# Optimization experiments

Hardware: AMD Instinct MI355X
Metric: run time of the kernel (lower is better)

## Reference

```python
import jax, jax.numpy as jnp
import numpy as np

WS = 16          # window_size
N = WS * WS      # tokens per window
H = 8            # num_heads
HD = 64          # head_dim
DIM = 512
EPEG_K = 15
PAD = EPEG_K // 2


def _relative_position_index(ws):
    coords = np.stack(np.meshgrid(np.arange(ws), np.arange(ws), indexing='ij'))  # (2, ws, ws)
    flat = coords.reshape(2, -1)                                                 # (2, N)
    rel = flat[:, :, None] - flat[:, None, :]                                    # (2, N, N)
    rel = rel.transpose(1, 2, 0).astype(np.int64)                                # (N, N, 2)
    rel[..., 0] += ws - 1
    rel[..., 1] += ws - 1
    rel[..., 0] *= 2 * ws - 1
    return rel.sum(-1)                                                           # (N, N)

REL_IDX = jnp.asarray(_relative_position_index(WS), dtype=jnp.int32)


def setup_inputs() -> dict:
    key = jax.random.key(0)
    ks = jax.random.split(key, 8)
    B_ = 128
    x = jax.random.normal(ks[0], (B_, N, DIM), dtype=jnp.float32)
    qkv_w = jax.random.normal(ks[1], (3 * H * HD, DIM), dtype=jnp.float32) * 0.02
    qkv_b = jnp.zeros((3 * H * HD,), dtype=jnp.float32)
    pe_w = jax.random.normal(ks[2], (H, 1, EPEG_K, 1), dtype=jnp.float32) * 0.02  # depthwise (15,1) conv
    pe_b = jnp.zeros((H,), dtype=jnp.float32)
    rpb_table = jax.random.normal(ks[3], ((2 * WS - 1) * (2 * WS - 1), H), dtype=jnp.float32) * 0.02
    proj_w = jax.random.normal(ks[4], (DIM, H * HD), dtype=jnp.float32) * 0.02
    proj_b = jnp.zeros((DIM,), dtype=jnp.float32)
    return {"x": x, "qkv_w": qkv_w, "qkv_b": qkv_b, "pe_w": pe_w, "pe_b": pe_b,
            "rpb_table": rpb_table, "proj_w": proj_w, "proj_b": proj_b}


def reference(x, qkv_w, qkv_b, pe_w, pe_b, rpb_table, proj_w, proj_b):
    B_, n, _ = x.shape
    scale = HD ** -0.5
    qkv = (x @ qkv_w.T + qkv_b).reshape(B_, n, 3, H, HD).transpose(2, 0, 3, 1, 4)  # (3,B_,H,N,hd)
    q, k, v = qkv[0] * scale, qkv[1], qkv[2]
    attn = jnp.einsum('bhnd,bhmd->bhnm', q, k)                                    # (B_,H,N,N)
    # epeg: depthwise conv (k,1) over the score map, per head
    pe = jax.lax.conv_general_dilated(
        attn, pe_w, window_strides=(1, 1), padding=((PAD, PAD), (0, 0)),
        dimension_numbers=('NCHW', 'OIHW', 'NCHW'), feature_group_count=H)
    attn = attn + pe + pe_b[None, :, None, None]
    bias = rpb_table[REL_IDX.reshape(-1)].reshape(n, n, H).transpose(2, 0, 1)     # (H,N,N)
    attn = jax.nn.softmax(attn + bias[None], axis=-1)
    out = jnp.einsum('bhnm,bhmd->bnhd', attn, v).reshape(B_, n, H * HD)
    return out @ proj_w.T + proj_b
```

## Files before the change

kernel.cpp:

```cpp
#include <hip/hip_runtime.h>


typedef unsigned short u16;
typedef unsigned int u32;
typedef __attribute__((ext_vector_type(8))) short short8;
typedef __attribute__((ext_vector_type(4))) float f32x4;

__device__ __forceinline__ u16 f2bf(float f) {
  union { float f; u32 u; } v; v.f = f;
  return (u16)((v.u + 0x7FFFu + ((v.u >> 16) & 1u)) >> 16);
}
__device__ __forceinline__ float bf2f(u16 s) {
  union { u32 u; float f; } v; v.u = ((u32)s) << 16;
  return v.f;
}
__device__ __forceinline__ u32 cvtpk(float lo, float hi) {
  u32 r;
  asm("v_cvt_pk_bf16_f32 %0, %1, %2" : "=v"(r) : "v"(lo), "v"(hi));
  return r;
}

__device__ __forceinline__ void gl2lds16(const u16* g, u16* l) {
  __builtin_amdgcn_global_load_lds((const __attribute__((address_space(1))) void*)g,
                                   (__attribute__((address_space(3))) void*)l, 16, 0, 0);
}

__device__ __forceinline__ int fragaddr(int frag, int lane) {
  return (frag * 64 + (lane ^ (frag & 7))) * 8;
}

__global__ __launch_bounds__(256) void cvt_all(
    const float* __restrict__ x, const float* __restrict__ w1f,
    const float* __restrict__ w2f, u16* __restrict__ xo,
    u16* __restrict__ w1o, u16* __restrict__ w2o) {
  const int NX = 4194304, NW1 = 196608, NW2 = 65536;
  int i = blockIdx.x * 256 + threadIdx.x;
  const float* src; u16* dst; int j;
  if (i < NX)                  { src = x;   dst = xo;  j = i; }
  else if (i < NX + NW1)       { src = w1f; dst = w1o; j = i - NX; }
  else if (i < NX + NW1 + NW2) { src = w2f; dst = w2o; j = i - NX - NW1; }
  else return;
  float4 f = ((const float4*)src)[j];
  uint2 o;
  o.x = (u32)f2bf(f.x) | ((u32)f2bf(f.y) << 16);
  o.y = (u32)f2bf(f.z) | ((u32)f2bf(f.w) << 16);
  ((uint2*)dst)[j] = o;
}

__device__ __forceinline__ void gemm256_core(
    const u16* __restrict__ A, const u16* __restrict__ B,
    int m0, int n0, u16* lds, f32x4 acc[8][4]) {
  const int NT = 8;
  int tid = threadIdx.x, wave = tid >> 6, lane = tid & 63;
  int wm = wave >> 2, wn = wave & 3;

  int ch0 = tid, ch1 = tid + 512;
  int row0 = ch0 >> 2, row1 = ch1 >> 2;
  int cg0 = (ch0 & 3) ^ (row0 & 3) ^ ((row0 >> 2) & 3);
  int cg1 = (ch1 & 3) ^ (row1 & 3) ^ ((row1 >> 2) & 3);
  const u16* Ag0 = A + (size_t)(m0 + row0) * 512 + cg0 * 8;
  const u16* Ag1 = A + (size_t)(m0 + row1) * 512 + cg1 * 8;
  const u16* Bg0 = B + (size_t)(n0 + row0) * 512 + cg0 * 8;
  const u16* Bg1 = B + (size_t)(n0 + row1) * 512 + cg1 * 8;
  int ldsu0 = wave * 64 * 8;
  int ldsu1 = (512 + wave * 64) * 8;

  int frag_off = (lane & 15) * 32 +
                 (((lane >> 4) ^ (lane & 3) ^ ((lane >> 2) & 3)) << 3);
  int abase = wm * 4096 + frag_off;
  int bbase = 8192 + wn * 2048 + frag_off;

#define STAGE(h)                                                             \
  do {                                                                       \
    if ((h) < NT * 4) {                                                      \
      int T_ = (h) >> 2, kh_ = ((h) >> 1) & 1, isB_ = (h) & 1;               \
      int ko_ = T_ * 64 + kh_ * 32;                                          \
      u16* d_ = lds + (T_ & 1) * 32768 + kh_ * 16384 + isB_ * 8192;          \
      gl2lds16((isB_ ? Bg0 : Ag0) + ko_, d_ + ldsu0);                        \
      gl2lds16((isB_ ? Bg1 : Ag1) + ko_, d_ + ldsu1);                        \
    }                                                                        \
  } while (0)

#define LDA(dst, mf, kh, p)                                                  \
  dst = *(const short8*)(lds + (p) * 32768 + (kh) * 16384 + abase + (mf) * 512)
#define LDB(dst, nf, kh, p)                                                  \
  dst = *(const short8*)(lds + (p) * 32768 + (kh) * 16384 + bbase + (nf) * 512)

#define MM16(M0)                                                                                   \
  __builtin_amdgcn_s_setprio(1);                                                                   \
  acc[(M0)+0][0] = __builtin_amdgcn_mfma_f32_16x16x32_bf16(b0, a0, acc[(M0)+0][0], 0, 0, 0);       \
  acc[(M0)+0][1] = __builtin_amdgcn_mfma_f32_16x16x32_bf16(b1, a0, acc[(M0)+0][1], 0, 0, 0);       \
  acc[(M0)+0][2] = __builtin_amdgcn_mfma_f32_16x16x32_bf16(b2, a0, acc[(M0)+0][2], 0, 0, 0);       \
  acc[(M0)+0][3] = __builtin_amdgcn_mfma_f32_16x16x32_bf16(b3, a0, acc[(M0)+0][3], 0, 0, 0);       \
  acc[(M0)+1][0] = __builtin_amdgcn_mfma_f32_16x16x32_bf16(b0, a1, acc[(M0)+1][0], 0, 0, 0);       \
  acc[(M0)+1][1] = __builtin_amdgcn_mfma_f32_16x16x32_bf16(b1, a1, acc[(M0)+1][1], 0, 0, 0);       \
  acc[(M0)+1][2] = __builtin_amdgcn_mfma_f32_16x16x32_bf16(b2, a1, acc[(M0)+1][2], 0, 0, 0);       \
  acc[(M0)+1][3] = __builtin_amdgcn_mfma_f32_16x16x32_bf16(b3, a1, acc[(M0)+1][3], 0, 0, 0);       \
  acc[(M0)+2][0] = __builtin_amdgcn_mfma_f32_16x16x32_bf16(b0, a2, acc[(M0)+2][0], 0, 0, 0);       \
  acc[(M0)+2][1] = __builtin_amdgcn_mfma_f32_16x16x32_bf16(b1, a2, acc[(M0)+2][1], 0, 0, 0);       \
  acc[(M0)+2][2] = __builtin_amdgcn_mfma_f32_16x16x32_bf16(b2, a2, acc[(M0)+2][2], 0, 0, 0);       \
  acc[(M0)+2][3] = __builtin_amdgcn_mfma_f32_16x16x32_bf16(b3, a2, acc[(M0)+2][3], 0, 0, 0);       \
  acc[(M0)+3][0] = __builtin_amdgcn_mfma_f32_16x16x32_bf16(b0, a3, acc[(M0)+3][0], 0, 0, 0);       \
  acc[(M0)+3][1] = __builtin_amdgcn_mfma_f32_16x16x32_bf16(b1, a3, acc[(M0)+3][1], 0, 0, 0);       \
  acc[(M0)+3][2] = __builtin_amdgcn_mfma_f32_16x16x32_bf16(b2, a3, acc[(M0)+3][2], 0, 0, 0);       \
  acc[(M0)+3][3] = __builtin_amdgcn_mfma_f32_16x16x32_bf16(b3, a3, acc[(M0)+3][3], 0, 0, 0);       \
  __builtin_amdgcn_s_setprio(0)

  STAGE(0); STAGE(1); STAGE(2); STAGE(3); STAGE(4);
  asm volatile("s_waitcnt vmcnt(6)" ::: "memory");
  __builtin_amdgcn_s_barrier();

#pragma unroll 1
  for (int kt = 0; kt < NT; ++kt) {
    int p = kt & 1;
    int hb = kt * 4 + 5;
    short8 a0, a1, a2, a3, b0, b1, b2, b3;
    LDA(a0, 0, 0, p); LDA(a1, 1, 0, p); LDA(a2, 2, 0, p); LDA(a3, 3, 0, p);
    LDB(b0, 0, 0, p); LDB(b1, 1, 0, p); LDB(b2, 2, 0, p); LDB(b3, 3, 0, p);
    STAGE(hb);
    __builtin_amdgcn_s_barrier();
    asm volatile("s_waitcnt lgkmcnt(0)" ::: "memory");
    MM16(0);
    __builtin_amdgcn_s_barrier();
    LDA(a0, 4, 0, p); LDA(a1, 5, 0, p); LDA(a2, 6, 0, p); LDA(a3, 7, 0, p);
    STAGE(hb + 1);
    __builtin_amdgcn_s_barrier();
    asm volatile("s_waitcnt lgkmcnt(0)" ::: "memory");
    MM16(4);
    if (kt == NT - 1) asm volatile("s_waitcnt vmcnt(0)" ::: "memory");
    else              asm volatile("s_waitcnt vmcnt(6)" ::: "memory");
    __builtin_amdgcn_s_barrier();
    LDA(a0, 0, 1, p); LDA(a1, 1, 1, p); LDA(a2, 2, 1, p); LDA(a3, 3, 1, p);
    LDB(b0, 0, 1, p); LDB(b1, 1, 1, p); LDB(b2, 2, 1, p); LDB(b3, 3, 1, p);
    STAGE(hb + 2);
    __builtin_amdgcn_s_barrier();
    asm volatile("s_waitcnt lgkmcnt(0)" ::: "memory");
    MM16(0);
    __builtin_amdgcn_s_barrier();
    LDA(a0, 4, 1, p); LDA(a1, 5, 1, p); LDA(a2, 6, 1, p); LDA(a3, 7, 1, p);
    STAGE(hb + 3);
    __builtin_amdgcn_s_barrier();
    asm volatile("s_waitcnt lgkmcnt(0)" ::: "memory");
    MM16(4);
    if (kt == NT - 2)     asm volatile("s_waitcnt vmcnt(4)" ::: "memory");
    else if (kt < NT - 2) asm volatile("s_waitcnt vmcnt(6)" ::: "memory");
    __builtin_amdgcn_s_barrier();
  }
#undef STAGE
#undef LDA
#undef LDB
#undef MM16
}

__global__ __launch_bounds__(512, 2) void gemm_qkv256(
    const u16* __restrict__ A, const u16* __restrict__ B,
    const float* __restrict__ qkvb, u16* __restrict__ qb,
    u16* __restrict__ kb, u16* __restrict__ vb) {
  __shared__ __align__(16) u16 lds[65536];
  f32x4 acc[8][4];
#pragma unroll
  for (int a = 0; a < 8; ++a)
#pragma unroll
    for (int c = 0; c < 4; ++c) acc[a][c] = (f32x4){0.f, 0.f, 0.f, 0.f};
  int bid = blockIdx.x;
  int wg = (bid & 7) * 96 + (bid >> 3);
  int m0 = (wg / 6) * 256, n0 = (wg % 6) * 256;
  gemm256_core(A, B, m0, n0, lds, acc);

  int tid = threadIdx.x, wave = tid >> 6, lane = tid & 63;
  int wm = wave >> 2, wn = wave & 3;
  int cx = lane & 15, g = lane >> 4;

  __syncthreads();
  float sc = (n0 < 512) ? 0.125f : 1.f;
  float4 bvn[4];
#pragma unroll
  for (int nf = 0; nf < 4; ++nf)
    bvn[nf] = *(const float4*)(qkvb + n0 + wn * 64 + nf * 16 + g * 4);
#pragma unroll
  for (int mf = 0; mf < 8; ++mf) {
    int r = wm * 128 + mf * 16 + cx;
    int swz = r & 7;
#pragma unroll
    for (int nf = 0; nf < 4; ++nf) {
      int c0 = wn * 64 + nf * 16 + g * 4;
      int c16 = (c0 >> 3) ^ swz;
      f32x4 v = acc[mf][nf];
      u32 w0 = cvtpk((v[0] + bvn[nf].x) * sc, (v[1] + bvn[nf].y) * sc);
      u32 w1 = cvtpk((v[2] + bvn[nf].z) * sc, (v[3] + bvn[nf].w) * sc);
      *(uint2*)(lds + r * 256 + c16 * 8 + (c0 & 7)) = make_uint2(w0, w1);
    }
  }
  __syncthreads();

  int b = m0 >> 8;
  int nrow = tid >> 3, dc = tid & 7;
#pragma unroll
  for (int j = 0; j < 16; ++j) {
    const int hg = j >> 2;
    int gcol = n0 + hg * 64;
    int which = gcol >> 9;
    int h = (gcol >> 6) & 7;
    u16* dst = (which == 0 ? qb : (which == 1 ? kb : vb)) +
               (size_t)(b * 8 + h) * 16384;
    int n = (j & 3) * 64 + nrow;
    int c16 = (hg * 8 + dc) ^ (n & 7);
    uint4 val = *(const uint4*)(lds + n * 256 + c16 * 8);
    *(uint4*)(dst + n * 64 + dc * 8) = val;
  }
}

__global__ __launch_bounds__(512, 2) void gemm_proj256(
    const u16* __restrict__ A, const u16* __restrict__ B,
    const float* __restrict__ pb, float* __restrict__ out) {
  __shared__ __align__(16) u16 lds[65536];
  f32x4 acc[8][4];
#pragma unroll
  for (int a = 0; a < 8; ++a)
#pragma unroll
    for (int c = 0; c < 4; ++c) acc[a][c] = (f32x4){0.f, 0.f, 0.f, 0.f};
  int bid = blockIdx.x;
  int wg = (bid & 7) * 32 + (bid >> 3);
  int m0 = (wg >> 1) * 256, n0 = (wg & 1) * 256;
  gemm256_core(A, B, m0, n0, lds, acc);

  int tid = threadIdx.x, wave = tid >> 6, lane = tid & 63;
  int wm = wave >> 2, wn = wave & 3;
  int cx = lane & 15, g = lane >> 4;
  int cb = n0 + wn * 64 + g * 4;
  float4 bv[4];
#pragma unroll
  for (int nf = 0; nf < 4; ++nf) bv[nf] = *(const float4*)(pb + cb + nf * 16);
  int r0 = m0 + wm * 128 + cx;
#pragma unroll
  for (int mf = 0; mf < 8; ++mf) {
    size_t rb = (size_t)(r0 + mf * 16) * 512;
#pragma unroll
    for (int nf = 0; nf < 4; ++nf) {
      f32x4 v = acc[mf][nf];
      float4 o = make_float4(v[0] + bv[nf].x, v[1] + bv[nf].y,
                             v[2] + bv[nf].z, v[3] + bv[nf].w);
      *(float4*)(out + rb + cb + nf * 16) = o;
    }
  }
}

__global__ __launch_bounds__(256) void qconv(u16* __restrict__ qb,
                                             const float* __restrict__ pe_w) {
  __shared__ __align__(16) u16 Ql[256 * 72];
  __shared__ float w[15];
  int bh = blockIdx.x, h = bh & 7, tid = threadIdx.x;
  const uint4* src = (const uint4*)(qb + (size_t)bh * 16384);
#pragma unroll
  for (int it = 0; it < 8; ++it) {
    int idx = tid + it * 256;
    int row = idx >> 3, c = (idx & 7) * 8;
    *(uint4*)(Ql + row * 72 + c) = src[idx];
  }
  if (tid < 15) w[tid] = pe_w[h * 15 + tid] + (tid == 7 ? 1.f : 0.f);
  __syncthreads();
  int dg = (tid & 15) * 4, nb4 = tid >> 4;
  uint2* dst = (uint2*)(qb + (size_t)bh * 16384);
#pragma unroll
  for (int i = 0; i < 16; ++i) {
    int n = nb4 + i * 16;
    float a0 = 0.f, a1 = 0.f, a2 = 0.f, a3 = 0.f;
#pragma unroll
    for (int t = 0; t < 15; ++t) {
      int nn = n + t - 7;
      if (nn < 0 || nn > 255) continue;
      uint2 rv = *(const uint2*)(Ql + nn * 72 + dg);
      float wt = w[t];
      a0 += wt * bf2f(rv.x & 0xffff); a1 += wt * bf2f(rv.x >> 16);
      a2 += wt * bf2f(rv.y & 0xffff); a3 += wt * bf2f(rv.y >> 16);
    }
    uint2 pv;
    pv.x = (u32)f2bf(a0) | ((u32)f2bf(a1) << 16);
    pv.y = (u32)f2bf(a2) | ((u32)f2bf(a3) << 16);
    dst[(n * 64 + dg) >> 2] = pv;
  }
}

__global__ __launch_bounds__(512, 2) void attn_win(
    const u16* __restrict__ qb, const u16* __restrict__ kb,
    const u16* __restrict__ vb, const float* __restrict__ pe_b,
    const float* __restrict__ rpb, u16* __restrict__ attnout) {
  __shared__ __align__(16) u16 KfPs[21504];
  __shared__ __align__(16) u16 Vf[16384];
  __shared__ float biasl[961];

  int bh = blockIdx.x, b = bh >> 3, h = bh & 7;
  int tid = threadIdx.x, wave = tid >> 6, lane = tid & 63;
  int cx = lane & 15, g = lane >> 4;

  const uint4* kg = (const uint4*)(kb + (size_t)bh * 16384);
  const uint4* vg = (const uint4*)(vb + (size_t)bh * 16384);
  const u16* qgb = qb + (size_t)bh * 16384;

  short8 qfr0a = *(const short8*)(qgb + (0 * 128 + wave * 16 + cx) * 64 + g * 8);
  short8 qfr0b = *(const short8*)(qgb + (0 * 128 + wave * 16 + cx) * 64 + 32 + g * 8);
  short8 qfr1a = *(const short8*)(qgb + (1 * 128 + wave * 16 + cx) * 64 + g * 8);
  short8 qfr1b = *(const short8*)(qgb + (1 * 128 + wave * 16 + cx) * 64 + 32 + g * 8);

  uint4 kreg[4];
#pragma unroll
  for (int it = 0; it < 4; ++it) kreg[it] = kg[tid + it * 512];

  u16* Vtmp = KfPs;
#pragma unroll
  for (int it = 0; it < 4; ++it) {
    int idx = tid + it * 512;
    uint4 v = vg[idx];
    int row = idx >> 3, c8 = (idx & 7) * 8;
    *(uint2*)(Vtmp + row * 68 + c8)     = make_uint2(v.x, v.y);
    *(uint2*)(Vtmp + row * 68 + c8 + 4) = make_uint2(v.z, v.w);
  }
  {
    float peb = pe_b[h];
    for (int i = tid; i < 961; i += 512) biasl[i] = rpb[i * 8 + h] + peb;
  }
  __syncthreads();

#pragma unroll
  for (int it = 0; it < 4; ++it) {
    int o = tid + it * 512;
    int frag = o >> 6, lanep = o & 63;
    int d = (frag >> 3) * 16 + (lanep & 15);
    int mb = (frag & 7) * 32 + (lanep >> 4) * 8;
    uint4 pk;
    pk.x = (u32)Vtmp[(mb + 0) * 68 + d] | ((u32)Vtmp[(mb + 1) * 68 + d] << 16);
    pk.y = (u32)Vtmp[(mb + 2) * 68 + d] | ((u32)Vtmp[(mb + 3) * 68 + d] << 16);
    pk.z = (u32)Vtmp[(mb + 4) * 68 + d] | ((u32)Vtmp[(mb + 5) * 68 + d] << 16);
    pk.w = (u32)Vtmp[(mb + 6) * 68 + d] | ((u32)Vtmp[(mb + 7) * 68 + d] << 16);
    *(uint4*)(Vf + (frag * 64 + (lanep ^ (frag & 7))) * 8) = pk;
  }
  __syncthreads();

  u16* Kf = KfPs;
#pragma unroll
  for (int it = 0; it < 4; ++it) {
    int idx = tid + it * 512;
    int n = idx >> 3, k8 = idx & 7;
    int frag = (n >> 4) * 2 + (k8 >> 2);
    int lanep = (n & 15) + 16 * (k8 & 3);
    *(uint4*)(Kf + (frag * 64 + (lanep ^ (frag & 7))) * 8) = kreg[it];
  }
  __syncthreads();

  u16* Psw = KfPs + 16384 + wave * 640;

#pragma unroll
  for (int it2 = 0; it2 < 2; ++it2) {
    short8 qf0 = it2 ? qfr1a : qfr0a;
    short8 qf1 = it2 ? qfr1b : qfr0b;
    int qbase = it2 * 128 + wave * 16;

    float m_run = -1e30f, l_run = 0.f;
    f32x4 oacc[4];
#pragma unroll
    for (int dt = 0; dt < 4; ++dt) oacc[dt] = (f32x4){0.f, 0.f, 0.f, 0.f};

#pragma unroll
    for (int c = 0; c < 2; ++c) {
      f32x4 acc[8];
#pragma unroll
      for (int mt = 0; mt < 8; ++mt) acc[mt] = (f32x4){0.f, 0.f, 0.f, 0.f};
      __builtin_amdgcn_s_setprio(1);
#pragma unroll
      for (int mt = 0; mt < 8; ++mt) {
        int fr = (c * 8 + mt) * 2;
        short8 k0 = *(const short8*)(Kf + fragaddr(fr, lane));
        short8 k1 = *(const short8*)(Kf + fragaddr(fr + 1, lane));
        acc[mt] = __builtin_amdgcn_mfma_f32_16x16x32_bf16(k0, qf0, acc[mt], 0, 0, 0);
        acc[mt] = __builtin_amdgcn_mfma_f32_16x16x32_bf16(k1, qf1, acc[mt], 0, 0, 0);
      }
      __builtin_amdgcn_s_setprio(0);

      int nb = (it2 * 8 + wave - c * 8 + 15) * 31 + cx - g * 4 + 15;
#pragma unroll
      for (int mt = 0; mt < 8; ++mt) {
        const float* bp = biasl + (nb - 31 * mt);
        acc[mt][0] += bp[0];  acc[mt][1] += bp[-1];
        acc[mt][2] += bp[-2]; acc[mt][3] += bp[-3];
      }

      float mx = fmaxf(fmaxf(acc[0][0], acc[0][1]), fmaxf(acc[0][2], acc[0][3]));
#pragma unroll
      for (int mt = 1; mt < 8; ++mt)
        mx = fmaxf(mx, fmaxf(fmaxf(acc[mt][0], acc[mt][1]),
                             fmaxf(acc[mt][2], acc[mt][3])));
      mx = fmaxf(mx, __shfl_xor(mx, 16));
      mx = fmaxf(mx, __shfl_xor(mx, 32));
      float mnew = fmaxf(m_run, mx);
      float al = __expf(m_run - mnew);
      float s = 0.f;
#pragma unroll
      for (int mt = 0; mt < 8; ++mt)
#pragma unroll
        for (int i = 0; i < 4; ++i) {
          float e = __expf(acc[mt][i] - mnew);
          acc[mt][i] = e; s += e;
        }
      s += __shfl_xor(s, 16);
      s += __shfl_xor(s, 32);
      l_run = l_run * al + s;
      m_run = mnew;

#pragma unroll
      for (int dt = 0; dt < 4; ++dt)
#pragma unroll
        for (int i = 0; i < 4; ++i) oacc[dt][i] *= al;

#pragma unroll
      for (int kk = 0; kk < 4; ++kk) {
        u32 w0 = cvtpk(acc[2 * kk][0], acc[2 * kk][1]);
        u32 w1 = cvtpk(acc[2 * kk][2], acc[2 * kk][3]);
        u32 w2 = cvtpk(acc[2 * kk + 1][0], acc[2 * kk + 1][1]);
        u32 w3 = cvtpk(acc[2 * kk + 1][2], acc[2 * kk + 1][3]);
        *(uint2*)(Psw + cx * 40 + g * 4)      = make_uint2(w0, w1);
        *(uint2*)(Psw + cx * 40 + 16 + g * 4) = make_uint2(w2, w3);
        short8 pa = *(const short8*)(Psw + cx * 40 + g * 8);
        __builtin_amdgcn_s_setprio(1);
#pragma unroll
        for (int dt = 0; dt < 4; ++dt) {
          short8 vf = *(const short8*)(Vf + fragaddr(dt * 8 + c * 4 + kk, lane));
          oacc[dt] = __builtin_amdgcn_mfma_f32_16x16x32_bf16(vf, pa, oacc[dt], 0, 0, 0);
        }
        __builtin_amdgcn_s_setprio(0);
      }
    }

    float inv = 1.f / l_run;
    u16* ao = attnout + ((size_t)b * 256 + qbase + cx) * 512 + h * 64;
#pragma unroll
    for (int dt = 0; dt < 4; ++dt) {
      u32 w0 = cvtpk(oacc[dt][0] * inv, oacc[dt][1] * inv);
      u32 w1 = cvtpk(oacc[dt][2] * inv, oacc[dt][3] * inv);
      *(uint2*)(ao + dt * 16 + g * 4) = make_uint2(w0, w1);
    }
  }
}

extern "C" void kernel_launch(void* const* d_in, const int* in_sizes, int n_in,
                              void* d_out, int out_size, void* d_ws, size_t ws_size,
                              hipStream_t stream) {
  const float* x      = (const float*)d_in[0];
  const float* qkv_w  = (const float*)d_in[1];
  const float* qkv_b  = (const float*)d_in[2];
  const float* pe_w   = (const float*)d_in[3];
  const float* pe_b   = (const float*)d_in[4];
  const float* rpb    = (const float*)d_in[5];
  const float* proj_w = (const float*)d_in[6];
  const float* proj_b = (const float*)d_in[7];
  float* out = (float*)d_out;
  char* ws = (char*)d_ws;

  size_t off = 0;
  u16* xbf = (u16*)(ws + off); off += (size_t)16777216 * 2;
  u16* w1  = (u16*)(ws + off); off += (size_t)786432 * 2;
  u16* w2  = (u16*)(ws + off); off += (size_t)262144 * 2;
  u16* qb  = (u16*)(ws + off); off += (size_t)16777216 * 2;
  u16* kb  = (u16*)(ws + off); off += (size_t)16777216 * 2;
  u16* vb  = (u16*)(ws + off); off += (size_t)16777216 * 2;

  hipLaunchKernelGGL(cvt_all, dim3(17408), dim3(256), 0, stream,
                     x, qkv_w, proj_w, xbf, w1, w2);
  hipLaunchKernelGGL(gemm_qkv256, dim3(768), dim3(512), 0, stream,
                     xbf, w1, qkv_b, qb, kb, vb);
  hipLaunchKernelGGL(qconv, dim3(1024), dim3(256), 0, stream, qb, pe_w);
  hipLaunchKernelGGL(attn_win, dim3(1024), dim3(512), 0, stream,
                     qb, kb, vb, pe_b, rpb, xbf);
  hipLaunchKernelGGL(gemm_proj256, dim3(256), dim3(512), 0, stream,
                     xbf, w2, proj_b, out);
}
```

Baseline: 303.3 us.

## Fuse Q-side conv into attention kernel prologue via shared memory

Removes the separate qconv kernel, which read Q from global memory, applied the 15-tap conv with an identity tap, and wrote it back. The attention kernel now stages Q in shared memory (reusing the K/P buffer), applies the conv there and builds the Q MFMA fragments from shared memory. This drops one launch and a full read-write round trip of Q through global memory. In exchange it adds several barriers and a conv prologue to every attention block, which lengthens the prologue and raises register pressure.

```diff
diff --git a/kernel.cpp b/kernel.cpp
--- a/kernel.cpp
+++ b/kernel.cpp
@@ -245,66 +245,75 @@
   }
 }
 
-__global__ __launch_bounds__(256) void qconv(u16* __restrict__ qb,
-                                             const float* __restrict__ pe_w) {
-  __shared__ __align__(16) u16 Ql[256 * 72];
-  __shared__ float w[15];
-  int bh = blockIdx.x, h = bh & 7, tid = threadIdx.x;
-  const uint4* src = (const uint4*)(qb + (size_t)bh * 16384);
-#pragma unroll
-  for (int it = 0; it < 8; ++it) {
-    int idx = tid + it * 256;
+__global__ __launch_bounds__(512, 2) void attn_win(
+    const u16* __restrict__ qb, const u16* __restrict__ kb,
+    const u16* __restrict__ vb, const float* __restrict__ pe_w,
+    const float* __restrict__ pe_b, const float* __restrict__ rpb,
+    u16* __restrict__ attnout) {
+  __shared__ __align__(16) u16 KfPs[21504];
+  __shared__ __align__(16) u16 Vf[16384];
+  __shared__ float biasl[961];
+  __shared__ float wsh[15];
+
+  int bh = blockIdx.x, b = bh >> 3, h = bh & 7;
+  int tid = threadIdx.x, wave = tid >> 6, lane = tid & 63;
+  int cx = lane & 15, g = lane >> 4;
+
+  const uint4* kg = (const uint4*)(kb + (size_t)bh * 16384);
+  const uint4* vg = (const uint4*)(vb + (size_t)bh * 16384);
+  const uint4* qg = (const uint4*)(qb + (size_t)bh * 16384);
+
+  uint4 kreg[4];
+#pragma unroll
+  for (int it = 0; it < 4; ++it) kreg[it] = kg[tid + it * 512];
+
+  u16* Ql = KfPs;
+#pragma unroll
+  for (int it = 0; it < 4; ++it) {
+    int idx = tid + it * 512;
     int row = idx >> 3, c = (idx & 7) * 8;
-    *(uint4*)(Ql + row * 72 + c) = src[idx];
-  }
-  if (tid < 15) w[tid] = pe_w[h * 15 + tid] + (tid == 7 ? 1.f : 0.f);
-  __syncthreads();
-  int dg = (tid & 15) * 4, nb4 = tid >> 4;
-  uint2* dst = (uint2*)(qb + (size_t)bh * 16384);
-#pragma unroll
-  for (int i = 0; i < 16; ++i) {
-    int n = nb4 + i * 16;
+    *(uint4*)(Ql + row * 72 + c) = qg[idx];
+  }
+  if (tid < 15) wsh[tid] = pe_w[h * 15 + tid] + (tid == 7 ? 1.f : 0.f);
+  {
+    float peb = pe_b[h];
+    for (int i = tid; i < 961; i += 512) biasl[i] = rpb[i * 8 + h] + peb;
+  }
+  __syncthreads();
+
+  int dg = (tid & 15) * 4, nb = tid >> 4;
+  float ca[8][4];
+#pragma unroll
+  for (int i = 0; i < 8; ++i) {
+    int n = nb + i * 32;
     float a0 = 0.f, a1 = 0.f, a2 = 0.f, a3 = 0.f;
 #pragma unroll
     for (int t = 0; t < 15; ++t) {
       int nn = n + t - 7;
       if (nn < 0 || nn > 255) continue;
       uint2 rv = *(const uint2*)(Ql + nn * 72 + dg);
-      float wt = w[t];
+      float wt = wsh[t];
       a0 += wt * bf2f(rv.x & 0xffff); a1 += wt * bf2f(rv.x >> 16);
       a2 += wt * bf2f(rv.y & 0xffff); a3 += wt * bf2f(rv.y >> 16);
     }
+    ca[i][0] = a0; ca[i][1] = a1; ca[i][2] = a2; ca[i][3] = a3;
+  }
+  __syncthreads();
+#pragma unroll
+  for (int i = 0; i < 8; ++i) {
+    int n = nb + i * 32;
     uint2 pv;
-    pv.x = (u32)f2bf(a0) | ((u32)f2bf(a1) << 16);
-    pv.y = (u32)f2bf(a2) | ((u32)f2bf(a3) << 16);
-    dst[(n * 64 + dg) >> 2] = pv;
-  }
-}
-
-__global__ __launch_bounds__(512, 2) void attn_win(
-    const u16* __restrict__ qb, const u16* __restrict__ kb,
-    const u16* __restrict__ vb, const float* __restrict__ pe_b,
-    const float* __restrict__ rpb, u16* __restrict__ attnout) {
-  __shared__ __align__(16) u16 KfPs[21504];
-  __shared__ __align__(16) u16 Vf[16384];
-  __shared__ float biasl[961];
-
-  int bh = blockIdx.x, b = bh >> 3, h = bh & 7;
-  int tid = threadIdx.x, wave = tid >> 6, lane = tid & 63;
-  int cx = lane & 15, g = lane >> 4;
-
-  const uint4* kg = (const uint4*)(kb + (size_t)bh * 16384);
-  const uint4* vg = (const uint4*)(vb + (size_t)bh * 16384);
-  const u16* qgb = qb + (size_t)bh * 16384;
-
-  short8 qfr0a = *(const short8*)(qgb + (0 * 128 + wave * 16 + cx) * 64 + g * 8);
-  short8 qfr0b = *(const short8*)(qgb + (0 * 128 + wave * 16 + cx) * 64 + 32 + g * 8);
-  short8 qfr1a = *(const short8*)(qgb + (1 * 128 + wave * 16 + cx) * 64 + g * 8);
-  short8 qfr1b = *(const short8*)(qgb + (1 * 128 + wave * 16 + cx) * 64 + 32 + g * 8);
-
-  uint4 kreg[4];
-#pragma unroll
-  for (int it = 0; it < 4; ++it) kreg[it] = kg[tid + it * 512];
+    pv.x = cvtpk(ca[i][0], ca[i][1]);
+    pv.y = cvtpk(ca[i][2], ca[i][3]);
+    *(uint2*)(Ql + n * 72 + dg) = pv;
+  }
+  __syncthreads();
+
+  short8 qfr0a = *(const short8*)(Ql + (0 * 128 + wave * 16 + cx) * 72 + g * 8);
+  short8 qfr0b = *(const short8*)(Ql + (0 * 128 + wave * 16 + cx) * 72 + 32 + g * 8);
+  short8 qfr1a = *(const short8*)(Ql + (1 * 128 + wave * 16 + cx) * 72 + g * 8);
+  short8 qfr1b = *(const short8*)(Ql + (1 * 128 + wave * 16 + cx) * 72 + 32 + g * 8);
+  __syncthreads();
 
   u16* Vtmp = KfPs;
 #pragma unroll
@@ -314,10 +323,6 @@
     int row = idx >> 3, c8 = (idx & 7) * 8;
     *(uint2*)(Vtmp + row * 68 + c8)     = make_uint2(v.x, v.y);
     *(uint2*)(Vtmp + row * 68 + c8 + 4) = make_uint2(v.z, v.w);
-  }
-  {
-    float peb = pe_b[h];
-    for (int i = tid; i < 961; i += 512) biasl[i] = rpb[i * 8 + h] + peb;
   }
   __syncthreads();
 
@@ -376,10 +381,10 @@
       }
       __builtin_amdgcn_s_setprio(0);
 
-      int nb = (it2 * 8 + wave - c * 8 + 15) * 31 + cx - g * 4 + 15;
+      int nb2 = (it2 * 8 + wave - c * 8 + 15) * 31 + cx - g * 4 + 15;
 #pragma unroll
       for (int mt = 0; mt < 8; ++mt) {
-        const float* bp = biasl + (nb - 31 * mt);
+        const float* bp = biasl + (nb2 - 31 * mt);
         acc[mt][0] += bp[0];  acc[mt][1] += bp[-1];
         acc[mt][2] += bp[-2]; acc[mt][3] += bp[-3];
       }
@@ -467,9 +472,8 @@
                      x, qkv_w, proj_w, xbf, w1, w2);
   hipLaunchKernelGGL(gemm_qkv256, dim3(768), dim3(512), 0, stream,
                      xbf, w1, qkv_b, qb, kb, vb);
-  hipLaunchKernelGGL(qconv, dim3(1024), dim3(256), 0, stream, qb, pe_w);
   hipLaunchKernelGGL(attn_win, dim3(1024), dim3(512), 0, stream,
-                     qb, kb, vb, pe_b, rpb, xbf);
+                     qb, kb, vb, pe_w, pe_b, rpb, xbf);
   hipLaunchKernelGGL(gemm_proj256, dim3(256), dim3(512), 0, stream,
                      xbf, w2, proj_b, out);
 }
```

Measured after the change: 309.6 us. +2.1%, slower.

## Feed softmax P directly from registers using 16x16x16 bf16 MFMA for PV

Applied to the files above, without the earlier changes.

The PV product switches from the 16x16x32 MFMA, which needed P staged through a per-wave LDS scratch buffer to reshape it, to the 16x16x16 bf16 MFMA. With that instruction the QK accumulator layout matches the operand layout, so P is packed in registers and used directly. The V fragment layout in LDS is rebuilt for 4-element k-slices, and the LDS buffer is shrunk because the P scratch is gone. This removes LDS write and read round-trips and the associated waits. In exchange it issues twice as many smaller MFMAs, which may have lower throughput per instruction.

```diff
diff --git a/kernel.cpp b/kernel.cpp
--- a/kernel.cpp
+++ b/kernel.cpp
@@ -4,6 +4,7 @@
 typedef unsigned short u16;
 typedef unsigned int u32;
 typedef __attribute__((ext_vector_type(8))) short short8;
+typedef __attribute__((ext_vector_type(4))) short s4b;
 typedef __attribute__((ext_vector_type(4))) float f32x4;
 
 __device__ __forceinline__ u16 f2bf(float f) {
@@ -18,6 +19,17 @@
   u32 r;
   asm("v_cvt_pk_bf16_f32 %0, %1, %2" : "=v"(r) : "v"(lo), "v"(hi));
   return r;
+}
+
+__device__ __forceinline__ f32x4 mfma16(s4b a, s4b b, f32x4 c) {
+#if __has_builtin(__builtin_amdgcn_mfma_f32_16x16x16bf16_1k)
+  return __builtin_amdgcn_mfma_f32_16x16x16bf16_1k(a, b, c, 0, 0, 0);
+#else
+  f32x4 d;
+  asm volatile("v_mfma_f32_16x16x16_bf16 %0, %1, %2, %3\n\ts_nop 4"
+               : "=v"(d) : "v"(a), "v"(b), "v"(c));
+  return d;
+#endif
 }
 
 __device__ __forceinline__ void gl2lds16(const u16* g, u16* l) {
@@ -285,7 +297,7 @@
     const u16* __restrict__ qb, const u16* __restrict__ kb,
     const u16* __restrict__ vb, const float* __restrict__ pe_b,
     const float* __restrict__ rpb, u16* __restrict__ attnout) {
-  __shared__ __align__(16) u16 KfPs[21504];
+  __shared__ __align__(16) u16 KfPs[17408];
   __shared__ __align__(16) u16 Vf[16384];
   __shared__ float biasl[961];
 
@@ -322,17 +334,15 @@
   __syncthreads();
 
 #pragma unroll
-  for (int it = 0; it < 4; ++it) {
+  for (int it = 0; it < 8; ++it) {
     int o = tid + it * 512;
     int frag = o >> 6, lanep = o & 63;
-    int d = (frag >> 3) * 16 + (lanep & 15);
-    int mb = (frag & 7) * 32 + (lanep >> 4) * 8;
-    uint4 pk;
+    int d = (frag >> 4) * 16 + (lanep & 15);
+    int mb = (frag & 15) * 16 + (lanep >> 4) * 4;
+    uint2 pk;
     pk.x = (u32)Vtmp[(mb + 0) * 68 + d] | ((u32)Vtmp[(mb + 1) * 68 + d] << 16);
     pk.y = (u32)Vtmp[(mb + 2) * 68 + d] | ((u32)Vtmp[(mb + 3) * 68 + d] << 16);
-    pk.z = (u32)Vtmp[(mb + 4) * 68 + d] | ((u32)Vtmp[(mb + 5) * 68 + d] << 16);
-    pk.w = (u32)Vtmp[(mb + 6) * 68 + d] | ((u32)Vtmp[(mb + 7) * 68 + d] << 16);
-    *(uint4*)(Vf + (frag * 64 + (lanep ^ (frag & 7))) * 8) = pk;
+    *(uint2*)(Vf + frag * 256 + lanep * 4) = pk;
   }
   __syncthreads();
 
@@ -346,8 +356,6 @@
     *(uint4*)(Kf + (frag * 64 + (lanep ^ (frag & 7))) * 8) = kreg[it];
   }
   __syncthreads();
-
-  u16* Psw = KfPs + 16384 + wave * 640;
 
 #pragma unroll
   for (int it2 = 0; it2 < 2; ++it2) {
@@ -376,10 +384,10 @@
       }
       __builtin_amdgcn_s_setprio(0);
 
-      int nb = (it2 * 8 + wave - c * 8 + 15) * 31 + cx - g * 4 + 15;
+      int nb2 = (it2 * 8 + wave - c * 8 + 15) * 31 + cx - g * 4 + 15;
 #pragma unroll
       for (int mt = 0; mt < 8; ++mt) {
-        const float* bp = biasl + (nb - 31 * mt);
+        const float* bp = biasl + (nb2 - 31 * mt);
         acc[mt][0] += bp[0];  acc[mt][1] += bp[-1];
         acc[mt][2] += bp[-2]; acc[mt][3] += bp[-3];
       }
@@ -412,19 +420,16 @@
         for (int i = 0; i < 4; ++i) oacc[dt][i] *= al;
 
 #pragma unroll
-      for (int kk = 0; kk < 4; ++kk) {
-        u32 w0 = cvtpk(acc[2 * kk][0], acc[2 * kk][1]);
-        u32 w1 = cvtpk(acc[2 * kk][2], acc[2 * kk][3]);
-        u32 w2 = cvtpk(acc[2 * kk + 1][0], acc[2 * kk + 1][1]);
-        u32 w3 = cvtpk(acc[2 * kk + 1][2], acc[2 * kk + 1][3]);
-        *(uint2*)(Psw + cx * 40 + g * 4)      = make_uint2(w0, w1);
-        *(uint2*)(Psw + cx * 40 + 16 + g * 4) = make_uint2(w2, w3);
-        short8 pa = *(const short8*)(Psw + cx * 40 + g * 8);
+      for (int mt = 0; mt < 8; ++mt) {
+        union { uint2 u; s4b s; } cv;
+        cv.u = make_uint2(cvtpk(acc[mt][0], acc[mt][1]),
+                          cvtpk(acc[mt][2], acc[mt][3]));
+        s4b pa = cv.s;
         __builtin_amdgcn_s_setprio(1);
 #pragma unroll
         for (int dt = 0; dt < 4; ++dt) {
-          short8 vf = *(const short8*)(Vf + fragaddr(dt * 8 + c * 4 + kk, lane));
-          oacc[dt] = __builtin_amdgcn_mfma_f32_16x16x32_bf16(vf, pa, oacc[dt], 0, 0, 0);
+          s4b vf = *(const s4b*)(Vf + (dt * 16 + c * 8 + mt) * 256 + lane * 4);
+          oacc[dt] = mfma16(vf, pa, oacc[dt]);
         }
         __builtin_amdgcn_s_setprio(0);
       }
```

Measured after the change: 300.2 us. Within noise of the previous version (-1.0%).
